# Optimization experiments

Measured on AMD Instinct MI355X. Metric: run time of the kernel, lower is better.

The kernel has to match this reference:

```python
import jax, jax.numpy as jnp
import numpy as np

BLOCK = 128
FP8_MAX = 448.0  # max finite value of float8_e4m3fn


def _quant_weight(w, key_unused=None):
    """Per-128x128-block FP8 quantization of weight [N, K].
    Returns (w_q_as_f32, scale[N//128, K//128])."""
    N, K = w.shape
    nb, kb = N // BLOCK, K // BLOCK
    wb = w.reshape(nb, BLOCK, kb, BLOCK)
    amax = jnp.max(jnp.abs(wb), axis=(1, 3))  # [nb, kb]
    scale = jnp.maximum(amax, 1e-12) / FP8_MAX
    w_q = (wb / scale[:, None, :, None]).astype(jnp.float8_e4m3fn).astype(jnp.float32)
    return w_q.reshape(N, K), scale.astype(jnp.float32)


def setup_inputs() -> dict:
    key = jax.random.key(0)
    k1, k2 = jax.random.split(key)
    B, S, K, N = 2, 2048, 7168, 4096
    x = jax.random.normal(k1, (B, S, K), dtype=jnp.float32)
    w_master = jax.random.normal(k2, (N, K), dtype=jnp.float32) * 0.02
    weight, weight_scale = _quant_weight(w_master)
    return {"x": x, "weight": weight, "weight_scale": weight_scale}


def act_quant(x):
    """Per-128-element block quant along last dim. Returns (x_q_f32, scale[..., K//128])."""
    *lead, K = x.shape
    kb = K // BLOCK
    xb = x.reshape(*lead, kb, BLOCK)
    amax = jnp.max(jnp.abs(xb), axis=-1)  # [..., kb]
    scale = jnp.maximum(amax, 1e-12) / FP8_MAX
    x_q = (xb / scale[..., None]).astype(jnp.float8_e4m3fn).astype(jnp.float32)
    return x_q.reshape(*lead, K), scale


def reference(x, weight, weight_scale):
    # 1) blockwise FP8 activation quant
    x_q, a_scale = act_quant(x)  # x_q: [B,S,K], a_scale: [B,S,K//128]
    # 2) dequant-equivalent GEMM: y[m,n] = sum_k x_q[m,k]*a_s[m,blk(k)] * w_q[n,k]*w_s[blk(n),blk(k)]
    x_deq = x_q * jnp.repeat(a_scale, BLOCK, axis=-1)  # [B,S,K]
    w_deq = weight * jnp.repeat(jnp.repeat(weight_scale, BLOCK, axis=0), BLOCK, axis=1)  # [N,K]
    y = jnp.einsum('bsk,nk->bsn', x_deq, w_deq)
    return y
```

## Files before the change

### kernel.cpp

```cpp
#include <hip/hip_runtime.h>

#define K_DIM 7168
#define N_DIM 4096
#define KBLKS 56
#define FP8MAX 448.0f
#define BM 256
#define BN 256

typedef float f32x4 __attribute__((ext_vector_type(4)));

#define GLOBAL_AS __attribute__((address_space(1)))
#define LDS_AS __attribute__((address_space(3)))

__device__ __forceinline__ void gload_lds16(const void* g, void* l) {
  __builtin_amdgcn_global_load_lds((GLOBAL_AS void*)g, (LDS_AS void*)l, 16, 0, 0);
}

__device__ __forceinline__ int pack_fp8x4(float a, float b, float c, float d) {
  int v = __builtin_amdgcn_cvt_pk_fp8_f32(a, b, 0, false);
  v = __builtin_amdgcn_cvt_pk_fp8_f32(c, d, v, true);
  return v;
}

__global__ void quant_fused(const float* __restrict__ x, const float* __restrict__ w,
                            unsigned char* __restrict__ xq, unsigned char* __restrict__ wq,
                            float* __restrict__ asT, int M, long nw4) {
  long gidx = (long)blockIdx.x * blockDim.x + threadIdx.x;
  if (gidx < nw4) {
    float4 v = *(const float4*)(w + gidx * 4);
    ((int*)wq)[gidx] = pack_fp8x4(v.x, v.y, v.z, v.w);
    return;
  }
  long t = gidx - nw4;
  int gid = (int)(t >> 5);
  int lane = (int)t & 31;
  if (gid >= M * KBLKS) return;
  int m = gid / KBLKS;
  int kb = gid - m * KBLKS;
  size_t off = (size_t)m * K_DIM + kb * 128 + lane * 4;
  float4 v = *(const float4*)(x + off);
  float amax = fmaxf(fmaxf(fabsf(v.x), fabsf(v.y)), fmaxf(fabsf(v.z), fabsf(v.w)));
#pragma unroll
  for (int d = 16; d; d >>= 1) amax = fmaxf(amax, __shfl_xor(amax, d));
  float scale = fmaxf(amax, 1e-12f) / FP8MAX;
  *(int*)(xq + off) = pack_fp8x4(v.x / scale, v.y / scale, v.z / scale, v.w / scale);
  if (lane == 0) asT[(size_t)kb * M + m] = scale;
}

__global__ __launch_bounds__(512, 2)
void gemm_fp8_blk(const unsigned char* __restrict__ xq,
                  const unsigned char* __restrict__ wq,
                  const float* __restrict__ asT,
                  const float* __restrict__ wscale,
                  float* __restrict__ out, int M) {
  __shared__ unsigned char ldsA[2][32768];
  __shared__ unsigned char ldsB[2][32768];
  __shared__ float ldsAS[2][256];

  const int bid = blockIdx.x;
  const int nbn = N_DIM / BN;
  const int per = (M / BM) * nbn >> 3;
  const int swz = (bid & 7) * per + (bid >> 3);
  const int m0 = (swz / nbn) * BM, n0 = (swz % nbn) * BN;

  const int tid = threadIdx.x;
  const int wv = tid >> 6, lane = tid & 63;
  const int wm = (wv >> 2) * 128;
  const int wn = (wv & 3) * 64;
  const int rsel = lane & 15;
  const int ks = lane >> 4;
  const int j0 = ks >> 1, h8 = (ks & 1) * 8;
  const int jrow = ks * 4;

  int swk[4];
#pragma unroll
  for (int kk = 0; kk < 4; ++kk)
    swk[kk] = (((kk * 2 + j0) ^ (rsel & 7)) * 16) + h8;

  int srow[4], scol[4];
#pragma unroll
  for (int it = 0; it < 4; ++it) {
    int o = it * 8192 + wv * 1024 + lane * 16;
    int r = o >> 7, sl = (o >> 4) & 7;
    srow[it] = r;
    scol[it] = (sl ^ (r & 7)) * 16;
  }

  f32x4 acc[8][4] = {};

  auto stageA = [&](int t1, int b, int it) {
    gload_lds16(xq + (size_t)(m0 + srow[it]) * K_DIM + (size_t)t1 * 128 + scol[it],
                &ldsA[b][it * 8192 + wv * 1024]);
  };
  auto stageB = [&](int t1, int b, int it) {
    gload_lds16(wq + (size_t)(n0 + srow[it]) * K_DIM + (size_t)t1 * 128 + scol[it],
                &ldsB[b][it * 8192 + wv * 1024]);
  };
  auto stageS = [&](int t1, int b) {
    if (wv == 0) gload_lds16(asT + (size_t)t1 * M + m0 + lane * 4, &ldsAS[b][0]);
  };

#pragma unroll
  for (int it = 0; it < 4; ++it) { stageA(0, 0, it); stageB(0, 0, it); }
  stageS(0, 0);
  asm volatile("s_waitcnt vmcnt(0)" ::: "memory");
  __builtin_amdgcn_s_barrier();

  for (int t = 0; t < KBLKS; ++t) {
    const int cur = t & 1;
    const unsigned char* pA0 = &ldsA[cur][(wm + rsel) * 128];
    const unsigned char* pB0 = &ldsB[cur][(wn + rsel) * 128];
    const float wsv = wscale[(size_t)((n0 + wn) >> 7) * KBLKS + t];
    const bool pf = (t + 1 < KBLKS);

#pragma unroll
    for (int mh = 0; mh < 2; ++mh) {
#pragma unroll
      for (int nh = 0; nh < 2; ++nh) {
        f32x4 tmp[4][2];
#pragma unroll
        for (int kh = 0; kh < 2; ++kh) {
          const int p = mh * 4 + nh * 2 + kh;
          long a[4][2], b[2][2];
#pragma unroll
          for (int mi = 0; mi < 4; ++mi)
#pragma unroll
            for (int q = 0; q < 2; ++q)
              a[mi][q] = *(const long*)(pA0 + mh * 8192 + mi * 2048 + swk[kh * 2 + q]);
#pragma unroll
          for (int ni = 0; ni < 2; ++ni)
#pragma unroll
            for (int q = 0; q < 2; ++q)
              b[ni][q] = *(const long*)(pB0 + nh * 4096 + ni * 2048 + swk[kh * 2 + q]);

          if (pf) {
            if (p == 0) { stageA(t + 1, cur ^ 1, 0); stageA(t + 1, cur ^ 1, 1); stageS(t + 1, cur ^ 1); }
            if (p == 1) { stageA(t + 1, cur ^ 1, 2); stageA(t + 1, cur ^ 1, 3); }
            if (p == 2) { stageB(t + 1, cur ^ 1, 0); stageB(t + 1, cur ^ 1, 1); }
            if (p == 3) { stageB(t + 1, cur ^ 1, 2); stageB(t + 1, cur ^ 1, 3); }
          }
          __builtin_amdgcn_s_barrier();
          __builtin_amdgcn_s_setprio(1);
#pragma unroll
          for (int mi = 0; mi < 4; ++mi)
#pragma unroll
            for (int ni = 0; ni < 2; ++ni) {
              f32x4 t4 = (kh == 0) ? (f32x4){0.f, 0.f, 0.f, 0.f} : tmp[mi][ni];
              t4 = __builtin_amdgcn_mfma_f32_16x16x32_fp8_fp8(a[mi][0], b[ni][0], t4, 0, 0, 0);
              t4 = __builtin_amdgcn_mfma_f32_16x16x32_fp8_fp8(a[mi][1], b[ni][1], t4, 0, 0, 0);
              tmp[mi][ni] = t4;
            }
          __builtin_amdgcn_s_setprio(0);
          __builtin_amdgcn_s_barrier();
        }
        const float* pAS = &ldsAS[cur][wm + mh * 64 + jrow];
#pragma unroll
        for (int mi = 0; mi < 4; ++mi) {
          f32x4 as4 = *(const f32x4*)(pAS + mi * 16);
          f32x4 comb = as4 * wsv;
#pragma unroll
          for (int ni = 0; ni < 2; ++ni)
            acc[mh * 4 + mi][nh * 2 + ni] += tmp[mi][ni] * comb;
        }
      }
    }
    asm volatile("s_waitcnt vmcnt(0)" ::: "memory");
    __builtin_amdgcn_s_barrier();
  }

#pragma unroll
  for (int mi = 0; mi < 8; ++mi) {
#pragma unroll
    for (int j = 0; j < 4; ++j) {
      float* op = out + (size_t)(m0 + wm + mi * 16 + jrow + j) * N_DIM + n0 + wn + rsel;
#pragma unroll
      for (int ni = 0; ni < 4; ++ni) op[ni * 16] = acc[mi][ni][j];
    }
  }
}

extern "C" void kernel_launch(void* const* d_in, const int* in_sizes, int n_in,
                              void* d_out, int out_size, void* d_ws, size_t ws_size,
                              hipStream_t stream) {
  const float* x   = (const float*)d_in[0];
  const float* wgt = (const float*)d_in[1];
  const float* wsc = (const float*)d_in[2];
  float* out = (float*)d_out;

  const int K = K_DIM, N = N_DIM;
  const int M = in_sizes[0] / K;

  unsigned char* xq = (unsigned char*)d_ws;
  unsigned char* wq = xq + (size_t)M * K;
  float* asT = (float*)(wq + (size_t)N * K);

  long nw4 = (long)N * K / 4;
  long nx  = (long)M * KBLKS * 32;
  long tot = nw4 + nx;
  quant_fused<<<(int)((tot + 255) / 256), 256, 0, stream>>>(x, wgt, xq, wq, asT, M, nw4);

  dim3 grid((M / BM) * (N / BN));
  gemm_fp8_blk<<<grid, 512, 0, stream>>>(xq, wq, asT, wsc, out, M);
}
```

Baseline: 543.8 us.

## Reorganize LDS tiles into MFMA fragment order and drop inner-loop barriers

The GEMM's shared-memory layout changes from row-major swizzled tiles to a fragment-ordered layout, so each lane reads contiguous 8-byte fragments with a small XOR swizzle. The K-step is restructured: all B fragments are loaded once, the loop walks 8 M-subtiles with 4 chained MFMAs each, and the per-phase barriers and setprio are removed. Prefetch of the next K-block is issued up front in one batch instead of being interleaved across phases. The activation quant also switches from division to multiplication by a reciprocal, which may change rounding slightly. Holding B fragments and larger unrolled bodies in registers raises VGPR pressure and may spill under launch_bounds(512,2).

```diff
diff --git a/kernel.cpp b/kernel.cpp
--- a/kernel.cpp
+++ b/kernel.cpp
@@ -42,8 +42,10 @@
   float amax = fmaxf(fmaxf(fabsf(v.x), fabsf(v.y)), fmaxf(fabsf(v.z), fabsf(v.w)));
 #pragma unroll
   for (int d = 16; d; d >>= 1) amax = fmaxf(amax, __shfl_xor(amax, d));
-  float scale = fmaxf(amax, 1e-12f) / FP8MAX;
-  *(int*)(xq + off) = pack_fp8x4(v.x / scale, v.y / scale, v.z / scale, v.w / scale);
+  float am = fmaxf(amax, 1e-12f);
+  float scale = am / FP8MAX;
+  float inv = FP8MAX / am;
+  *(int*)(xq + off) = pack_fp8x4(v.x * inv, v.y * inv, v.z * inv, v.w * inv);
   if (lane == 0) asT[(size_t)kb * M + m] = scale;
 }
 
@@ -67,103 +69,74 @@
   const int wv = tid >> 6, lane = tid & 63;
   const int wm = (wv >> 2) * 128;
   const int wn = (wv & 3) * 64;
-  const int rsel = lane & 15;
-  const int ks = lane >> 4;
-  const int j0 = ks >> 1, h8 = (ks & 1) * 8;
-  const int jrow = ks * 4;
-
-  int swk[4];
-#pragma unroll
-  for (int kk = 0; kk < 4; ++kk)
-    swk[kk] = (((kk * 2 + j0) ^ (rsel & 7)) * 16) + h8;
+  const int rf = lane & 15, gf = lane >> 4;
+  const int jrow = gf * 4;
+  const int fragoff = rf * 32 + ((gf ^ ((((rf >> 2) & 1)) << 1))) * 8;
 
   int srow[4], scol[4];
 #pragma unroll
-  for (int it = 0; it < 4; ++it) {
-    int o = it * 8192 + wv * 1024 + lane * 16;
-    int r = o >> 7, sl = (o >> 4) & 7;
-    srow[it] = r;
-    scol[it] = (sl ^ (r & 7)) * 16;
+  for (int j = 0; j < 4; ++j) {
+    int c = wv * 256 + j * 64 + lane;
+    int mi = c >> 7, kk = (c >> 5) & 3, r = (c >> 1) & 15, h = c & 1;
+    srow[j] = mi * 16 + r;
+    scol[j] = kk * 32 + ((h ^ ((r >> 2) & 1)) << 4);
   }
 
   f32x4 acc[8][4] = {};
+  const f32x4 z4 = {0.f, 0.f, 0.f, 0.f};
 
-  auto stageA = [&](int t1, int b, int it) {
-    gload_lds16(xq + (size_t)(m0 + srow[it]) * K_DIM + (size_t)t1 * 128 + scol[it],
-                &ldsA[b][it * 8192 + wv * 1024]);
-  };
-  auto stageB = [&](int t1, int b, int it) {
-    gload_lds16(wq + (size_t)(n0 + srow[it]) * K_DIM + (size_t)t1 * 128 + scol[it],
-                &ldsB[b][it * 8192 + wv * 1024]);
-  };
-  auto stageS = [&](int t1, int b) {
+  auto stage = [&](int t1, int b) {
+#pragma unroll
+    for (int j = 0; j < 4; ++j)
+      gload_lds16(xq + (size_t)(m0 + srow[j]) * K_DIM + t1 * 128 + scol[j],
+                  &ldsA[b][wv * 4096 + j * 1024]);
+#pragma unroll
+    for (int j = 0; j < 4; ++j)
+      gload_lds16(wq + (size_t)(n0 + srow[j]) * K_DIM + t1 * 128 + scol[j],
+                  &ldsB[b][wv * 4096 + j * 1024]);
     if (wv == 0) gload_lds16(asT + (size_t)t1 * M + m0 + lane * 4, &ldsAS[b][0]);
   };
 
-#pragma unroll
-  for (int it = 0; it < 4; ++it) { stageA(0, 0, it); stageB(0, 0, it); }
-  stageS(0, 0);
+  stage(0, 0);
   asm volatile("s_waitcnt vmcnt(0)" ::: "memory");
   __builtin_amdgcn_s_barrier();
 
+  const int wsbase = ((n0 + wn) >> 7) * KBLKS;
+
   for (int t = 0; t < KBLKS; ++t) {
     const int cur = t & 1;
-    const unsigned char* pA0 = &ldsA[cur][(wm + rsel) * 128];
-    const unsigned char* pB0 = &ldsB[cur][(wn + rsel) * 128];
-    const float wsv = wscale[(size_t)((n0 + wn) >> 7) * KBLKS + t];
-    const bool pf = (t + 1 < KBLKS);
+    if (t + 1 < KBLKS) stage(t + 1, cur ^ 1);
+
+    const unsigned char* pA = &ldsA[cur][(wm >> 4) * 2048 + fragoff];
+    const unsigned char* pB = &ldsB[cur][(wv & 3) * 8192 + fragoff];
+    const float wsv = wscale[wsbase + t];
+    const float* pAS = &ldsAS[cur][wm + jrow];
+
+    long bfr[4][4];
+#pragma unroll
+    for (int ni = 0; ni < 4; ++ni)
+#pragma unroll
+      for (int kk = 0; kk < 4; ++kk)
+        bfr[ni][kk] = *(const long*)(pB + ni * 2048 + kk * 512);
 
 #pragma unroll
-    for (int mh = 0; mh < 2; ++mh) {
+    for (int mi = 0; mi < 8; ++mi) {
+      long af[4];
 #pragma unroll
-      for (int nh = 0; nh < 2; ++nh) {
-        f32x4 tmp[4][2];
+      for (int kk = 0; kk < 4; ++kk)
+        af[kk] = *(const long*)(pA + mi * 2048 + kk * 512);
+      f32x4 as4 = *(const f32x4*)(pAS + mi * 16);
+      f32x4 comb = as4 * wsv;
 #pragma unroll
-        for (int kh = 0; kh < 2; ++kh) {
-          const int p = mh * 4 + nh * 2 + kh;
-          long a[4][2], b[2][2];
-#pragma unroll
-          for (int mi = 0; mi < 4; ++mi)
-#pragma unroll
-            for (int q = 0; q < 2; ++q)
-              a[mi][q] = *(const long*)(pA0 + mh * 8192 + mi * 2048 + swk[kh * 2 + q]);
-#pragma unroll
-          for (int ni = 0; ni < 2; ++ni)
-#pragma unroll
-            for (int q = 0; q < 2; ++q)
-              b[ni][q] = *(const long*)(pB0 + nh * 4096 + ni * 2048 + swk[kh * 2 + q]);
-
-          if (pf) {
-            if (p == 0) { stageA(t + 1, cur ^ 1, 0); stageA(t + 1, cur ^ 1, 1); stageS(t + 1, cur ^ 1); }
-            if (p == 1) { stageA(t + 1, cur ^ 1, 2); stageA(t + 1, cur ^ 1, 3); }
-            if (p == 2) { stageB(t + 1, cur ^ 1, 0); stageB(t + 1, cur ^ 1, 1); }
-            if (p == 3) { stageB(t + 1, cur ^ 1, 2); stageB(t + 1, cur ^ 1, 3); }
-          }
-          __builtin_amdgcn_s_barrier();
-          __builtin_amdgcn_s_setprio(1);
-#pragma unroll
-          for (int mi = 0; mi < 4; ++mi)
-#pragma unroll
-            for (int ni = 0; ni < 2; ++ni) {
-              f32x4 t4 = (kh == 0) ? (f32x4){0.f, 0.f, 0.f, 0.f} : tmp[mi][ni];
-              t4 = __builtin_amdgcn_mfma_f32_16x16x32_fp8_fp8(a[mi][0], b[ni][0], t4, 0, 0, 0);
-              t4 = __builtin_amdgcn_mfma_f32_16x16x32_fp8_fp8(a[mi][1], b[ni][1], t4, 0, 0, 0);
-              tmp[mi][ni] = t4;
-            }
-          __builtin_amdgcn_s_setprio(0);
-          __builtin_amdgcn_s_barrier();
-        }
-        const float* pAS = &ldsAS[cur][wm + mh * 64 + jrow];
-#pragma unroll
-        for (int mi = 0; mi < 4; ++mi) {
-          f32x4 as4 = *(const f32x4*)(pAS + mi * 16);
-          f32x4 comb = as4 * wsv;
-#pragma unroll
-          for (int ni = 0; ni < 2; ++ni)
-            acc[mh * 4 + mi][nh * 2 + ni] += tmp[mi][ni] * comb;
-        }
+      for (int ni = 0; ni < 4; ++ni) {
+        f32x4 tp = __builtin_amdgcn_mfma_f32_16x16x32_fp8_fp8(af[0], bfr[ni][0], z4, 0, 0, 0);
+        tp = __builtin_amdgcn_mfma_f32_16x16x32_fp8_fp8(af[1], bfr[ni][1], tp, 0, 0, 0);
+        tp = __builtin_amdgcn_mfma_f32_16x16x32_fp8_fp8(af[2], bfr[ni][2], tp, 0, 0, 0);
+        tp = __builtin_amdgcn_mfma_f32_16x16x32_fp8_fp8(af[3], bfr[ni][3], tp, 0, 0, 0);
+        acc[mi][ni] += tp * comb;
       }
     }
+
     asm volatile("s_waitcnt vmcnt(0)" ::: "memory");
     __builtin_amdgcn_s_barrier();
   }
@@ -172,7 +145,7 @@
   for (int mi = 0; mi < 8; ++mi) {
 #pragma unroll
     for (int j = 0; j < 4; ++j) {
-      float* op = out + (size_t)(m0 + wm + mi * 16 + jrow + j) * N_DIM + n0 + wn + rsel;
+      float* op = out + (size_t)(m0 + wm + mi * 16 + jrow + j) * N_DIM + n0 + wn + rf;
 #pragma unroll
       for (int ni = 0; ni < 4; ++ni) op[ni * 16] = acc[mi][ni][j];
     }
```

Result: faster. 487.3 us (-10.4%).
